# Kernel optimization log

Hardware: AMD Instinct MI355X
Metric: run time of the kernel (lower is better)

Reference implementation:

```python
import jax, jax.numpy as jnp
import numpy as np

INPUT_SIZE = 416.0
CONF_THRESH = 0.25
IOU_THRESH = 0.45
N = 8192


def setup_inputs() -> dict:
    key = jax.random.key(0)
    preds = jax.random.normal(key, (1, 5, N), dtype=jnp.float32)
    return {"preds": preds}


def _pairwise_iou(b):
    # b: [N,4] xyxy -> iou: [N,N], matching the torch clamp(min=0) semantics
    xx1 = jnp.maximum(b[:, None, 0], b[None, :, 0])
    yy1 = jnp.maximum(b[:, None, 1], b[None, :, 1])
    xx2 = jnp.minimum(b[:, None, 2], b[None, :, 2])
    yy2 = jnp.minimum(b[:, None, 3], b[None, :, 3])
    inter = jnp.clip(xx2 - xx1, 0.0) * jnp.clip(yy2 - yy1, 0.0)
    area = jnp.clip(b[:, 2] - b[:, 0], 0.0) * jnp.clip(b[:, 3] - b[:, 1], 0.0)  # [N]
    union = area[:, None] + area[None, :] - inter
    return jnp.where(union > 0, inter / union, 0.0)


def reference(preds):
    # decode: preds [1,5,N] rows = (cx, cy, w, h, obj)
    p = preds[0].T  # [N,5]
    cx, cy, pw, ph, obj = p[:, 0], p[:, 1], p[:, 2], p[:, 3], p[:, 4]
    x1 = cx - pw * 0.5
    y1 = cy - ph * 0.5
    x2 = cx + pw * 0.5
    y2 = cy + ph * 0.5
    boxes = jnp.stack([x1, y1, x2, y2], axis=1)  # [N,4]
    scores = obj
    classes = jnp.zeros_like(scores)

    valid = scores > CONF_THRESH  # conf filter (kept as mask; invalid boxes never kept)
    # scale to absolute coords iff all coords are normalized (max <= 1)
    scale = jnp.where(jnp.max(boxes) <= 1.0, INPUT_SIZE, 1.0)
    boxes_abs = boxes * scale

    # greedy NMS over score-descending order
    order = jnp.argsort(-scores)
    b = boxes_abs[order]          # [N,4]
    s = scores[order]             # [N]
    v = valid[order]              # [N]
    c = classes[order]            # [N]

    iou = _pairwise_iou(b)        # [N,N]

    def step(suppressed, xs):
        iou_row, v_i, i = xs
        keep_i = v_i & jnp.logical_not(suppressed[i])
        suppressed = suppressed | (keep_i & (iou_row > IOU_THRESH))
        return suppressed, keep_i

    _, keep = jax.lax.scan(
        step,
        jnp.zeros((N,), dtype=bool),
        (iou, v, jnp.arange(N)),
    )  # keep: [N] bool, in sorted order

    out = jnp.stack(
        [b[:, 0] / INPUT_SIZE, b[:, 1] / INPUT_SIZE,
         b[:, 2] / INPUT_SIZE, b[:, 3] / INPUT_SIZE, s, c],
        axis=1,
    )  # [N,6]
    # fixed-shape jit-compatible output: suppressed/filtered rows are zeroed;
    # kept rows appear in descending-score order (same order torch compacts to)
    return jnp.where(keep[:, None], out, 0.0)
```

## Files before the change

kernel.cpp:

```cpp
#include <hip/hip_runtime.h>
#include <stdint.h>

typedef unsigned long long u64;
typedef unsigned int u32;

#define NBOX 8192
#define ACMAX 1024
#define NCH 16
#define CONF 0.25f
#define IOU_T 0.45f

#define OFF_CX1    256
#define OFF_CY1    (OFF_CX1 + ACMAX * 4)
#define OFF_CX2    (OFF_CX1 + 2 * ACMAX * 4)
#define OFF_CY2    (OFF_CX1 + 3 * ACMAX * 4)
#define OFF_CSC    (OFF_CX1 + 4 * ACMAX * 4)
#define OFF_CAR    (OFF_CX1 + 5 * ACMAX * 4)
#define OFF_ROFC   (OFF_CX1 + 6 * ACMAX * 4)
#define OFF_CMASKT (OFF_CX1 + 7 * ACMAX * 4)

__device__ inline u64 readlane64(u64 v, int l) {
    u32 lo = (u32)__builtin_amdgcn_readlane((int)(u32)v, l);
    u32 hi = (u32)__builtin_amdgcn_readlane((int)(u32)(v >> 32), l);
    return ((u64)hi << 32) | (u64)lo;
}

__device__ inline u32 encf(float f) {
    u32 u = __float_as_uint(f);
    return (u & 0x80000000u) ? ~u : (u | 0x80000000u);
}

__global__ void __launch_bounds__(1024) k_sort(
        const float* __restrict__ p,
        float* __restrict__ cx1, float* __restrict__ cy1,
        float* __restrict__ cx2, float* __restrict__ cy2,
        float* __restrict__ csc, float* __restrict__ car,
        int* __restrict__ rofc, float* __restrict__ out) {
    #pragma clang fp contract(off)
    int t = threadIdx.x;
    int b = blockIdx.x;
    __shared__ u64 keys[1024];
    __shared__ u32 accs[128][36];
    __shared__ u32 accs2[8][32];
    __shared__ float redm[16];
    __shared__ float s_gmax;

    int il4 = (t & 7) * 4;
    int js  = t >> 3;
    int ibase = b * 32;

    u64 Ki[4];
    #pragma unroll
    for (int q = 0; q < 4; q++) {
        int i = ibase + il4 + q;
        u32 e = encf(p[4 * NBOX + i]);
        Ki[q] = ((u64)e << 32) | ((u64)(8191 - i) << 19) | 0x1FFFFull;
    }

    u32 acc[4] = {0u, 0u, 0u, 0u};
    float mloc = -3.4e38f;
    for (int w = 0; w < 8; w++) {
        int j = w * 1024 + t;
        float cxj = p[j], cyj = p[NBOX + j];
        float pwj = p[2 * NBOX + j], phj = p[3 * NBOX + j];
        float sj = p[4 * NBOX + j];
        float hx = pwj * 0.5f, hy = phj * 0.5f;
        float x1 = cxj - hx, y1 = cyj - hy, x2 = cxj + hx, y2 = cyj + hy;
        bool act = (sj > CONF) && (x2 > x1) && (y2 > y1);
        mloc = fmaxf(mloc, fmaxf(fmaxf(x1, y1), fmaxf(x2, y2)));
        u32 e = encf(sj);
        u32 mult = act ? 65537u : 1u;
        __syncthreads();
        keys[t] = ((u64)e << 32) | ((u64)(8191 - j) << 19) | (u64)mult;
        __syncthreads();
        int base = js * 8;
        #pragma unroll
        for (int k2 = 0; k2 < 4; k2++) {
            u64 ka = keys[base + k2 * 2];
            u64 kb = keys[base + k2 * 2 + 1];
            u32 ma = (u32)ka & 0x1FFFFu;
            u32 mb = (u32)kb & 0x1FFFFu;
            #pragma unroll
            for (int q = 0; q < 4; q++) {
                acc[q] += (ka > Ki[q]) ? ma : 0u;
                acc[q] += (kb > Ki[q]) ? mb : 0u;
            }
        }
    }
    #pragma unroll
    for (int q = 0; q < 4; q++) accs[js][il4 + q] = acc[q];
    #pragma unroll
    for (int o = 32; o > 0; o >>= 1) mloc = fmaxf(mloc, __shfl_xor(mloc, o, 64));
    if ((t & 63) == 0) redm[t >> 6] = mloc;
    __syncthreads();
    if (t < 256) {
        int il = t & 31, part = t >> 5;
        u32 s = 0;
        #pragma unroll
        for (int q = 0; q < 16; q++) s += accs[part * 16 + q][il];
        accs2[part][il] = s;
    }
    if (t == 0) {
        float g = redm[0];
        #pragma unroll
        for (int k = 1; k < 16; k++) g = fmaxf(g, redm[k]);
        s_gmax = g;
    }
    __syncthreads();
    if (t < 32) {
        u32 total = 0;
        #pragma unroll
        for (int part = 0; part < 8; part++) total += accs2[part][t];
        int r = (int)(total & 0xFFFFu);
        int cr = (int)(total >> 16);
        int i = ibase + t;
        float scale = (s_gmax <= 1.0f) ? 416.0f : 1.0f;
        float cx = p[i], cy = p[NBOX + i];
        float pw = p[2 * NBOX + i], ph = p[3 * NBOX + i];
        float s = p[4 * NBOX + i];
        float hx = pw * 0.5f, hy = ph * 0.5f;
        float x1 = cx - hx, y1 = cy - hy, x2 = cx + hx, y2 = cy + hy;
        bool a = (s > CONF) && (x2 > x1) && (y2 > y1);
        float bx1 = x1 * scale, by1 = y1 * scale;
        float bx2 = x2 * scale, by2 = y2 * scale;
        float aw = fmaxf(bx2 - bx1, 0.0f);
        float ah = fmaxf(by2 - by1, 0.0f);
        float area = aw * ah;
        bool ok = a && (cr < ACMAX);
        if (ok) {
            cx1[cr] = bx1; cy1[cr] = by1; cx2[cr] = bx2; cy2[cr] = by2;
            csc[cr] = s; car[cr] = area; rofc[cr] = r;
        } else {
            bool valid = s > CONF;
            float* o = out + (size_t)r * 6;
            o[0] = valid ? bx1 / 416.0f : 0.0f;
            o[1] = valid ? by1 / 416.0f : 0.0f;
            o[2] = valid ? bx2 / 416.0f : 0.0f;
            o[3] = valid ? by2 / 416.0f : 0.0f;
            o[4] = valid ? s : 0.0f;
            o[5] = 0.0f;
        }
    }
}

__global__ void __launch_bounds__(64) k_mask(
        const float* __restrict__ cx1, const float* __restrict__ cy1,
        const float* __restrict__ cx2, const float* __restrict__ cy2,
        const float* __restrict__ car, const float* __restrict__ csc,
        u64* __restrict__ cmaskT) {
    #pragma clang fp contract(off)
    int t = threadIdx.x;
    int i0 = blockIdx.x * 64, j0 = blockIdx.y * 64;
    u64 rv = __ballot(csc[i0 + t] > CONF);
    u64 cv = __ballot(csc[j0 + t] > CONF);
    if (rv == 0ull || cv == 0ull) return;
    __shared__ float sx1[64], sy1[64], sx2[64], sy2[64], sa[64];
    sx1[t] = cx1[i0 + t]; sy1[t] = cy1[i0 + t];
    sx2[t] = cx2[i0 + t]; sy2[t] = cy2[i0 + t];
    sa[t] = car[i0 + t];
    __syncthreads();
    int j = j0 + t;
    float xj1 = cx1[j], yj1 = cy1[j], xj2 = cx2[j], yj2 = cy2[j], aj = car[j];
    u64 w = 0;
    for (int ii = 0; ii < 64; ii++) {
        float xx1 = fmaxf(sx1[ii], xj1);
        float yy1 = fmaxf(sy1[ii], yj1);
        float xx2 = fminf(sx2[ii], xj2);
        float yy2 = fminf(sy2[ii], yj2);
        float iw = fmaxf(xx2 - xx1, 0.0f);
        float ih = fmaxf(yy2 - yy1, 0.0f);
        float inter = iw * ih;
        float uni = sa[ii] + aj - inter;
        bool sup = (uni > 0.0f) && (inter / uni > IOU_T);
        w |= ((u64)(sup ? 1u : 0u)) << ii;
    }
    cmaskT[(size_t)blockIdx.x * ACMAX + j] = w;
}

__global__ void __launch_bounds__(1024) k_final(
        const float* __restrict__ csc, const u64* __restrict__ cmaskT,
        const float* __restrict__ cx1, const float* __restrict__ cy1,
        const float* __restrict__ cx2, const float* __restrict__ cy2,
        const int* __restrict__ rofc, float* __restrict__ out) {
    int t = threadIdx.x;
    __shared__ u64 keptArr[NCH];
    int wv = t >> 6;
    float s = csc[t];
    bool valid = s > CONF;
    u64 col[NCH];
    #pragma unroll
    for (int w = 0; w < NCH; w++) col[w] = cmaskT[(size_t)w * ACMAX + t];
    bool sup = false;
    for (int c = 0; c < NCH; c++) {
        if (wv == c) {
            u64 validm = __ballot(valid);
            u64 supm = __ballot(sup);
            u64 d = col[c];
            u64 kept = 0;
            u64 cand = validm & ~supm;
            while (cand) {
                int i = __builtin_ctzll(cand);
                kept |= (1ull << i);
                u64 row = readlane64(d, i);
                u64 gt = (i < 63) ? (~0ull << (i + 1)) : 0ull;
                cand = cand & ~row & gt;
            }
            if ((t & 63) == 0) keptArr[c] = kept;
        }
        __syncthreads();
        u64 k = keptArr[c];
        if (wv > c && (col[c] & k) != 0ull) sup = true;
    }
    __syncthreads();
    if (valid) {
        bool kb = (keptArr[t >> 6] >> (t & 63)) & 1ull;
        int r = rofc[t];
        float* o = out + (size_t)r * 6;
        o[0] = kb ? cx1[t] / 416.0f : 0.0f;
        o[1] = kb ? cy1[t] / 416.0f : 0.0f;
        o[2] = kb ? cx2[t] / 416.0f : 0.0f;
        o[3] = kb ? cy2[t] / 416.0f : 0.0f;
        o[4] = kb ? s : 0.0f;
        o[5] = 0.0f;
    }
}

extern "C" void kernel_launch(void* const* d_in, const int* in_sizes, int n_in,
                              void* d_out, int out_size, void* d_ws, size_t ws_size,
                              hipStream_t stream) {
    const float* preds = (const float*)d_in[0];
    float* out = (float*)d_out;
    char* ws = (char*)d_ws;
    float* cx1 = (float*)(ws + OFF_CX1);
    float* cy1 = (float*)(ws + OFF_CY1);
    float* cx2 = (float*)(ws + OFF_CX2);
    float* cy2 = (float*)(ws + OFF_CY2);
    float* csc = (float*)(ws + OFF_CSC);
    float* car = (float*)(ws + OFF_CAR);
    int* rofc  = (int*)(ws + OFF_ROFC);
    u64* cmaskT = (u64*)(ws + OFF_CMASKT);

    hipLaunchKernelGGL(k_sort, dim3(256), dim3(1024), 0, stream,
                       preds, cx1, cy1, cx2, cy2, csc, car, rofc, out);
    hipLaunchKernelGGL(k_mask, dim3(NCH, NCH), dim3(64), 0, stream,
                       cx1, cy1, cx2, cy2, car, csc, cmaskT);
    hipLaunchKernelGGL(k_final, dim3(1), dim3(1024), 0, stream,
                       csc, cmaskT, cx1, cy1, cx2, cy2, rofc, out);
}
```

Measured before the change: 102.0 us.

## Replace sequential chunked greedy NMS with parallel fixed-point iteration over kept masks

The final kernel no longer walks the 16 chunks one wave at a time with a serial per-bit loop. All waves now iterate together: each box recomputes whether any currently kept earlier box suppresses it, kept masks are updated, and the loop repeats until no mask changes (checked with __syncthreads_or). This removes the wave serialization and the dependent readlane chain. In exchange the number of iterations depends on the length of the suppression dependency chain, so it could be worse than the serial version in adversarial cases.

```diff
diff --git a/kernel.cpp b/kernel.cpp
--- a/kernel.cpp
+++ b/kernel.cpp
@@ -18,12 +18,6 @@
 #define OFF_CAR    (OFF_CX1 + 5 * ACMAX * 4)
 #define OFF_ROFC   (OFF_CX1 + 6 * ACMAX * 4)
 #define OFF_CMASKT (OFF_CX1 + 7 * ACMAX * 4)
-
-__device__ inline u64 readlane64(u64 v, int l) {
-    u32 lo = (u32)__builtin_amdgcn_readlane((int)(u32)v, l);
-    u32 hi = (u32)__builtin_amdgcn_readlane((int)(u32)(v >> 32), l);
-    return ((u64)hi << 32) | (u64)lo;
-}
 
 __device__ inline u32 encf(float f) {
     u32 u = __float_as_uint(f);
@@ -185,35 +179,29 @@
     int t = threadIdx.x;
     __shared__ u64 keptArr[NCH];
     int wv = t >> 6;
+    int j = t & 63;
     float s = csc[t];
     bool valid = s > CONF;
     u64 col[NCH];
     #pragma unroll
     for (int w = 0; w < NCH; w++) col[w] = cmaskT[(size_t)w * ACMAX + t];
-    bool sup = false;
-    for (int c = 0; c < NCH; c++) {
-        if (wv == c) {
-            u64 validm = __ballot(valid);
-            u64 supm = __ballot(sup);
-            u64 d = col[c];
-            u64 kept = 0;
-            u64 cand = validm & ~supm;
-            while (cand) {
-                int i = __builtin_ctzll(cand);
-                kept |= (1ull << i);
-                u64 row = readlane64(d, i);
-                u64 gt = (i < 63) ? (~0ull << (i + 1)) : 0ull;
-                cand = cand & ~row & gt;
-            }
-            if ((t & 63) == 0) keptArr[c] = kept;
-        }
+    u64 validm = __ballot(valid);
+    if (j == 0) keptArr[wv] = validm;
+    __syncthreads();
+    u64 below = (j == 0) ? 0ull : (~0ull >> (64 - j));
+    for (int iter = 0; iter < 1024; ++iter) {
+        bool sup = false;
+        for (int w = 0; w < wv; ++w)
+            sup |= (col[w] & keptArr[w]) != 0ull;
+        sup |= (col[wv] & keptArr[wv] & below) != 0ull;
+        u64 nk = validm & ~__ballot(sup);
+        int ch = (nk != keptArr[wv]) ? 1 : 0;
         __syncthreads();
-        u64 k = keptArr[c];
-        if (wv > c && (col[c] & k) != 0ull) sup = true;
-    }
-    __syncthreads();
+        if (j == 0) keptArr[wv] = nk;
+        if (!__syncthreads_or(ch)) break;
+    }
     if (valid) {
-        bool kb = (keptArr[t >> 6] >> (t & 63)) & 1ull;
+        bool kb = (keptArr[wv] >> j) & 1ull;
         int r = rofc[t];
         float* o = out + (size_t)r * 6;
         o[0] = kb ? cx1[t] / 416.0f : 0.0f;
```

New measurement: 94.30 us. 1.08x faster.
